# Kernel tuning notes

Measured on AMD Instinct MI355X. Metric: run time of the kernel, lower is better.

## Reference

```python
import jax, jax.numpy as jnp
import numpy as np

B, T, CODE_NUM, MED_NUM = 256, 32, 4880, 1000
CODE_SIZE, H, OUT = 128, 128, 4880


def setup_inputs() -> dict:
    key = jax.random.key(0)
    ks = jax.random.split(key, 16)
    code_x = (jax.random.uniform(ks[0], (B, T, CODE_NUM)) < 0.05).astype(jnp.float32)
    medicine_codes = (jax.random.uniform(ks[1], (B, T, MED_NUM)) < 0.02).astype(jnp.float32)
    divided = (jax.random.uniform(ks[2], (B, T, CODE_NUM)) < 0.05).astype(jnp.float32)
    neighbors = (jax.random.uniform(ks[3], (B, T, CODE_NUM)) < 0.05).astype(jnp.float32)
    lens = jax.random.randint(ks[4], (B,), 1, T + 1)
    s = lambda fan: 1.0 / np.sqrt(fan)
    c_emb = jax.random.normal(ks[5], (CODE_NUM, CODE_SIZE)) * s(CODE_SIZE)
    m_emb = jax.random.normal(ks[6], (MED_NUM, CODE_SIZE)) * s(CODE_SIZE)
    W_c = jax.random.normal(ks[7], (CODE_SIZE, H)) * s(CODE_SIZE)
    W_m = jax.random.normal(ks[8], (CODE_SIZE, H)) * s(CODE_SIZE)
    Wa = jax.random.normal(ks[9], (3 * H, 32)) * s(3 * H)
    ba = jnp.zeros((32,), jnp.float32)
    va = jax.random.normal(ks[10], (32,)) * s(32)
    W_cls = jax.random.normal(ks[11], (3 * H, OUT)) * s(3 * H)
    b_cls = jnp.zeros((OUT,), jnp.float32)
    return dict(code_x=code_x, divided=divided, neighbors=neighbors, lens=lens,
                medicine_codes=medicine_codes, c_emb=c_emb, m_emb=m_emb,
                W_c=W_c, W_m=W_m, Wa=Wa, ba=ba, va=va, W_cls=W_cls, b_cls=b_cls)


def _forward(code_x, medicine_codes, lens, c_emb, m_emb, W_c, W_m, Wa, ba, va, W_cls, b_cls):
    # hypergraph_part: transform code/med embeddings, aggregate active codes per visit
    Hc = jnp.tanh(c_emb @ W_c)                      # [code_num, H]
    Hm = jnp.tanh(m_emb @ W_m)                      # [med_num, H]
    sum_c = jnp.einsum('btc,ch->bth', code_x, Hc)   # masked sum over active dx codes
    sum_m = jnp.einsum('btm,mh->bth', medicine_codes, Hm)
    h_c = sum_c / jnp.clip(code_x.sum(-1, keepdims=True), 1.0, None)
    h_m = sum_m / jnp.clip(medicine_codes.sum(-1, keepdims=True), 1.0, None)
    repre = jnp.concatenate([h_c, h_m, h_c * h_m], axis=-1)  # [B,T,3H]
    # DotProductAttention over visits, masked by lens
    scores = jnp.einsum('btk,k->bt', jnp.tanh(repre @ Wa + ba), va)
    mask = jnp.arange(T)[None, :] < lens[:, None]
    attn = jax.nn.softmax(jnp.where(mask, scores, -1e9), axis=-1)
    ctx = jnp.einsum('bt,btd->bd', attn, repre)     # [B,3H]
    # Classifier (dropout=identity in eval) + sigmoid
    return jax.nn.sigmoid(ctx @ W_cls + b_cls)      # [B,OUT]


def reference(code_x, divided, neighbors, lens, medicine_codes, c_emb, m_emb,
              W_c, W_m, Wa, ba, va, W_cls, b_cls):
    # divided/neighbors feed the transition branch whose output is unused
    # in the original forward's final prediction path.
    return _forward(code_x, medicine_codes, lens, c_emb, m_emb,
                    W_c, W_m, Wa, ba, va, W_cls, b_cls)
```

## Files before the change

kernel.cpp:

```cpp
#include <hip/hip_runtime.h>
#include <hip/hip_bf16.h>
#include <math.h>

#define Bsz 256
#define Tn 32
#define CODEN 4880
#define MEDN 1000
#define Hdim 128
#define OUTN 4880
#define BT (Bsz*Tn)
#define R3H 384

__global__ __launch_bounds__(128) void k_emb(
    const float* __restrict__ c_emb, const float* __restrict__ m_emb,
    const float* __restrict__ W_c, const float* __restrict__ W_m,
    float* __restrict__ Hc, float* __restrict__ Hm) {
  int row = blockIdx.x;
  const float* emb; const float* W; float* out;
  if (row < CODEN) { emb = c_emb + (size_t)row * Hdim; W = W_c; out = Hc + (size_t)row * Hdim; }
  else { int r = row - CODEN; emb = m_emb + (size_t)r * Hdim; W = W_m; out = Hm + (size_t)r * Hdim; }
  __shared__ float e[Hdim];
  int h = threadIdx.x;
  e[h] = emb[h];
  __syncthreads();
  float acc = 0.f;
#pragma unroll 8
  for (int k = 0; k < Hdim; ++k) acc += e[k] * W[k * Hdim + h];
  out[h] = tanhf(acc);
}

#define MAXC 1024
#define MAXM 256

__global__ __launch_bounds__(256) void k_visit(
    const float* __restrict__ code_x, const float* __restrict__ med,
    const float* __restrict__ Hc, const float* __restrict__ Hm,
    const float* __restrict__ Wa, const float* __restrict__ ba,
    const float* __restrict__ va,
    float* __restrict__ repre, float* __restrict__ scores) {
  int bt = blockIdx.x;
  int tid = threadIdx.x;
  __shared__ int list_c[MAXC];
  __shared__ int list_m[MAXM];
  __shared__ int cnt_c, cnt_m;
  __shared__ float rep_s[R3H];
  __shared__ float red[256];
  if (tid == 0) { cnt_c = 0; cnt_m = 0; }
  __syncthreads();

  const float4* cx = (const float4*)(code_x + (size_t)bt * CODEN);
  for (int i = tid; i < CODEN / 4; i += 256) {
    float4 v = cx[i];
    if (v.x != 0.f) { int p = atomicAdd(&cnt_c, 1); if (p < MAXC) list_c[p] = 4*i; }
    if (v.y != 0.f) { int p = atomicAdd(&cnt_c, 1); if (p < MAXC) list_c[p] = 4*i+1; }
    if (v.z != 0.f) { int p = atomicAdd(&cnt_c, 1); if (p < MAXC) list_c[p] = 4*i+2; }
    if (v.w != 0.f) { int p = atomicAdd(&cnt_c, 1); if (p < MAXC) list_c[p] = 4*i+3; }
  }
  const float4* mx = (const float4*)(med + (size_t)bt * MEDN);
  for (int i = tid; i < MEDN / 4; i += 256) {
    float4 v = mx[i];
    if (v.x != 0.f) { int p = atomicAdd(&cnt_m, 1); if (p < MAXM) list_m[p] = 4*i; }
    if (v.y != 0.f) { int p = atomicAdd(&cnt_m, 1); if (p < MAXM) list_m[p] = 4*i+1; }
    if (v.z != 0.f) { int p = atomicAdd(&cnt_m, 1); if (p < MAXM) list_m[p] = 4*i+2; }
    if (v.w != 0.f) { int p = atomicAdd(&cnt_m, 1); if (p < MAXM) list_m[p] = 4*i+3; }
  }
  __syncthreads();
  int nc = cnt_c < MAXC ? cnt_c : MAXC;
  int nm = cnt_m < MAXM ? cnt_m : MAXM;

  int h = tid & 127, half = tid >> 7;
  float accC = 0.f;
#pragma unroll 2
  for (int j = half; j < nc; j += 2) accC += Hc[(size_t)list_c[j] * Hdim + h];
  float accM = 0.f;
#pragma unroll 2
  for (int j = half; j < nm; j += 2) accM += Hm[(size_t)list_m[j] * Hdim + h];

  red[tid] = accC;
  __syncthreads();
  float hc = 0.f, hm = 0.f;
  if (half == 0) hc = (red[h] + red[h + 128]) / fmaxf((float)nc, 1.f);
  __syncthreads();
  red[tid] = accM;
  __syncthreads();
  if (half == 0) {
    hm = (red[h] + red[h + 128]) / fmaxf((float)nm, 1.f);
    rep_s[h] = hc;
    rep_s[Hdim + h] = hm;
    rep_s[2 * Hdim + h] = hc * hm;
  }
  __syncthreads();

  float* rp = repre + (size_t)bt * R3H;
  for (int i = tid; i < R3H; i += 256) rp[i] = rep_s[i];

  int j = tid & 31, kc = tid >> 5;
  float p = 0.f;
  int k0 = kc * 48;
#pragma unroll 8
  for (int k = k0; k < k0 + 48; ++k) p += rep_s[k] * Wa[k * 32 + j];
  __syncthreads();
  red[tid] = p;
  __syncthreads();
  if (tid < 32) {
    float tot = 0.f;
#pragma unroll
    for (int c = 0; c < 8; ++c) tot += red[c * 32 + tid];
    float u = tanhf(tot + ba[tid]);
    float sv = u * va[tid];
#pragma unroll
    for (int off = 16; off >= 1; off >>= 1) sv += __shfl_down(sv, off, 32);
    if (tid == 0) scores[bt] = sv;
  }
}

__global__ __launch_bounds__(128) void k_ctx(
    const float* __restrict__ scores, const int* __restrict__ lens,
    const float* __restrict__ repre, float* __restrict__ ctx) {
  int b = blockIdx.x, tid = threadIdx.x;
  __shared__ float attn[Tn];
  int len = lens[b];
  if (tid < Tn) {
    float s = scores[b * Tn + tid];
    bool valid = tid < len;
    float sm = valid ? s : -1e30f;
    float m = sm;
#pragma unroll
    for (int off = 16; off >= 1; off >>= 1) m = fmaxf(m, __shfl_xor(m, off, 32));
    float e = valid ? expf(sm - m) : 0.f;
    float sum = e;
#pragma unroll
    for (int off = 16; off >= 1; off >>= 1) sum += __shfl_xor(sum, off, 32);
    attn[tid] = e / sum;
  }
  __syncthreads();
  const float* rp = repre + (size_t)b * Tn * R3H;
  for (int d = tid; d < R3H; d += 128) {
    float a = 0.f;
#pragma unroll
    for (int t = 0; t < Tn; ++t) a += attn[t] * rp[t * R3H + d];
    ctx[(size_t)b * R3H + d] = a;
  }
}

#define FMA4(A, s, w) { A.x += (s)*(w).x; A.y += (s)*(w).y; A.z += (s)*(w).z; A.w += (s)*(w).w; }

__global__ __launch_bounds__(256) void k_cls(
    const float* __restrict__ ctx, const float* __restrict__ W_cls,
    const float* __restrict__ b_cls, float* __restrict__ out) {
  __shared__ float cs_t[R3H * 8];
  int tid = threadIdx.x;
  int ob = blockIdx.x % 5;
  int b0 = (blockIdx.x / 5) * 8;
  for (int i = tid; i < R3H * 8; i += 256) {
    int k = i >> 3, r = i & 7;
    cs_t[i] = ctx[(size_t)(b0 + r) * R3H + k];
  }
  __syncthreads();
  int o0 = ob * 1024 + tid * 4;
  if (o0 >= OUTN) return;
  float4 acc[8];
#pragma unroll
  for (int r = 0; r < 8; ++r) acc[r] = make_float4(0.f, 0.f, 0.f, 0.f);
  const float* wp = W_cls + o0;
#pragma unroll 2
  for (int k = 0; k < R3H; ++k) {
    float4 w = *(const float4*)(wp + (size_t)k * OUTN);
    float4 cA = *(const float4*)&cs_t[k * 8];
    float4 cB = *(const float4*)&cs_t[k * 8 + 4];
    FMA4(acc[0], cA.x, w); FMA4(acc[1], cA.y, w);
    FMA4(acc[2], cA.z, w); FMA4(acc[3], cA.w, w);
    FMA4(acc[4], cB.x, w); FMA4(acc[5], cB.y, w);
    FMA4(acc[6], cB.z, w); FMA4(acc[7], cB.w, w);
  }
  float4 bc = *(const float4*)(b_cls + o0);
#pragma unroll
  for (int r = 0; r < 8; ++r) {
    float4 v;
    v.x = 1.f / (1.f + expf(-(acc[r].x + bc.x)));
    v.y = 1.f / (1.f + expf(-(acc[r].y + bc.y)));
    v.z = 1.f / (1.f + expf(-(acc[r].z + bc.z)));
    v.w = 1.f / (1.f + expf(-(acc[r].w + bc.w)));
    *(float4*)(out + (size_t)(b0 + r) * OUTN + o0) = v;
  }
}

extern "C" void kernel_launch(void* const* d_in, const int* in_sizes, int n_in,
                              void* d_out, int out_size, void* d_ws, size_t ws_size,
                              hipStream_t stream) {
  const float* code_x = (const float*)d_in[0];
  const int*   lens   = (const int*)d_in[3];
  const float* med    = (const float*)d_in[4];
  const float* c_emb  = (const float*)d_in[5];
  const float* m_emb  = (const float*)d_in[6];
  const float* W_c    = (const float*)d_in[7];
  const float* W_m    = (const float*)d_in[8];
  const float* Wa     = (const float*)d_in[9];
  const float* ba     = (const float*)d_in[10];
  const float* va     = (const float*)d_in[11];
  const float* W_cls  = (const float*)d_in[12];
  const float* b_cls  = (const float*)d_in[13];
  float* out = (float*)d_out;
  float* ws  = (float*)d_ws;

  float* Hc     = ws;
  float* Hm     = ws + 624640;
  float* repre  = ws + 752640;
  float* scores = ws + 3898368;
  float* ctx    = ws + 3906560;

  hipLaunchKernelGGL(k_emb,   dim3(CODEN + MEDN), dim3(128), 0, stream,
                     c_emb, m_emb, W_c, W_m, Hc, Hm);
  hipLaunchKernelGGL(k_visit, dim3(BT), dim3(256), 0, stream,
                     code_x, med, Hc, Hm, Wa, ba, va, repre, scores);
  hipLaunchKernelGGL(k_ctx,   dim3(Bsz), dim3(128), 0, stream,
                     scores, lens, repre, ctx);
  hipLaunchKernelGGL(k_cls,   dim3(160), dim3(256), 0, stream,
                     ctx, W_cls, b_cls, out);
}
```

Measured before the change: 606.5 us.

## Replace sparse gather aggregation with fused bf16 MFMA dense GEMM per batch

Instead of building per-visit active-index lists and gathering Hc/Hm rows, each batch block computes code_x @ Hc and med @ Hm as dense bf16 MFMA GEMMs. The transposed bf16 embedding tiles are double-buffered through LDS with global_load_lds. The visit representation, attention scores, softmax and context are fused into the same kernel, which drops the repre/scores round-trip and the separate ctx kernel. The classifier loop also batches eight weight loads per step. This trades the sparsity exploitation for dense matrix-core throughput. Precision drops to bf16 for Hc/Hm, and only 256 blocks of one wave-group each run, so occupancy is limited.

```diff
diff --git a/kernel.cpp b/kernel.cpp
--- a/kernel.cpp
+++ b/kernel.cpp
@@ -8,142 +8,221 @@
 #define MEDN 1000
 #define Hdim 128
 #define OUTN 4880
-#define BT (Bsz*Tn)
 #define R3H 384
+#define KC_PAD 4896
+#define KM_PAD 1024
+#define NSC 153
+#define NSM 32
+
+typedef unsigned short u16;
+typedef __attribute__((ext_vector_type(4))) float f32x4;
+typedef __attribute__((ext_vector_type(8))) short s16x8;
+typedef __attribute__((ext_vector_type(4))) unsigned int u32x4;
+
+union PKU { u32x4 u; s16x8 s; };
+
+__device__ inline unsigned f2bf(float f) {
+  unsigned u = __float_as_uint(f);
+  return (u + 0x7fffu + ((u >> 16) & 1u)) >> 16;
+}
+__device__ inline unsigned pack2(float f0, float f1) {
+  return (__float_as_uint(f0) >> 16) | (__float_as_uint(f1) & 0xffff0000u);
+}
 
 __global__ __launch_bounds__(128) void k_emb(
     const float* __restrict__ c_emb, const float* __restrict__ m_emb,
     const float* __restrict__ W_c, const float* __restrict__ W_m,
-    float* __restrict__ Hc, float* __restrict__ Hm) {
-  int row = blockIdx.x;
-  const float* emb; const float* W; float* out;
-  if (row < CODEN) { emb = c_emb + (size_t)row * Hdim; W = W_c; out = Hc + (size_t)row * Hdim; }
-  else { int r = row - CODEN; emb = m_emb + (size_t)r * Hdim; W = W_m; out = Hm + (size_t)r * Hdim; }
+    u16* __restrict__ HcT, u16* __restrict__ HmT) {
+  int blk = blockIdx.x, h = threadIdx.x;
+  bool is_med = blk >= KC_PAD;
+  int c = is_med ? blk - KC_PAD : blk;
+  int n = is_med ? MEDN : CODEN;
+  u16* dst = is_med ? (HmT + (size_t)h * KM_PAD + c) : (HcT + (size_t)h * KC_PAD + c);
+  if (c >= n) { *dst = 0; return; }
+  const float* emb = (is_med ? m_emb : c_emb) + (size_t)c * Hdim;
+  const float* W = is_med ? W_m : W_c;
   __shared__ float e[Hdim];
-  int h = threadIdx.x;
   e[h] = emb[h];
   __syncthreads();
   float acc = 0.f;
 #pragma unroll 8
   for (int k = 0; k < Hdim; ++k) acc += e[k] * W[k * Hdim + h];
-  out[h] = tanhf(acc);
-}
-
-#define MAXC 1024
-#define MAXM 256
-
-__global__ __launch_bounds__(256) void k_visit(
+  *dst = (u16)f2bf(tanhf(acc));
+}
+
+__device__ inline void stageB(const u16* __restrict__ Bt, int k0, int ldk,
+                              u16* buf, int ttid) {
+#pragma unroll
+  for (int it = 0; it < 4; ++it) {
+    int c = it * 128 + ttid;
+    const u16* src = Bt + (size_t)(c & 127) * ldk + k0 + (c >> 7) * 8;
+#if __has_builtin(__builtin_amdgcn_global_load_lds)
+    __builtin_amdgcn_global_load_lds(
+        (const __attribute__((address_space(1))) void*)src,
+        (__attribute__((address_space(3))) void*)(buf + c * 8), 16, 0, 0);
+#else
+    *(u32x4*)(buf + c * 8) = *(const u32x4*)src;
+#endif
+  }
+}
+
+__device__ inline void loadA(const float* __restrict__ Arow, int kb, int kmax,
+                             float4& a0, float4& a1) {
+  if (kb < kmax) {
+    a0 = *(const float4*)(Arow + kb);
+    a1 = *(const float4*)(Arow + kb + 4);
+  } else {
+    a0 = make_float4(0.f, 0.f, 0.f, 0.f);
+    a1 = a0;
+  }
+}
+
+__global__ __launch_bounds__(256, 1) void k_agg(
     const float* __restrict__ code_x, const float* __restrict__ med,
-    const float* __restrict__ Hc, const float* __restrict__ Hm,
+    const u16* __restrict__ HcT, const u16* __restrict__ HmT,
     const float* __restrict__ Wa, const float* __restrict__ ba,
-    const float* __restrict__ va,
-    float* __restrict__ repre, float* __restrict__ scores) {
-  int bt = blockIdx.x;
+    const float* __restrict__ va, const int* __restrict__ lens,
+    float* __restrict__ ctx) {
+  __shared__ u16 Bc[2][4096];
+  __shared__ u16 Bm[2][4096];
+  __shared__ float Wa_s[R3H * 32];
+  __shared__ float rep_s[Tn][R3H + 4];
+  __shared__ float sc_s[Tn];
+  __shared__ float at_s[Tn];
+
+  int b = blockIdx.x;
   int tid = threadIdx.x;
-  __shared__ int list_c[MAXC];
-  __shared__ int list_m[MAXM];
-  __shared__ int cnt_c, cnt_m;
-  __shared__ float rep_s[R3H];
-  __shared__ float red[256];
-  if (tid == 0) { cnt_c = 0; cnt_m = 0; }
-  __syncthreads();
-
-  const float4* cx = (const float4*)(code_x + (size_t)bt * CODEN);
-  for (int i = tid; i < CODEN / 4; i += 256) {
-    float4 v = cx[i];
-    if (v.x != 0.f) { int p = atomicAdd(&cnt_c, 1); if (p < MAXC) list_c[p] = 4*i; }
-    if (v.y != 0.f) { int p = atomicAdd(&cnt_c, 1); if (p < MAXC) list_c[p] = 4*i+1; }
-    if (v.z != 0.f) { int p = atomicAdd(&cnt_c, 1); if (p < MAXC) list_c[p] = 4*i+2; }
-    if (v.w != 0.f) { int p = atomicAdd(&cnt_c, 1); if (p < MAXC) list_c[p] = 4*i+3; }
-  }
-  const float4* mx = (const float4*)(med + (size_t)bt * MEDN);
-  for (int i = tid; i < MEDN / 4; i += 256) {
-    float4 v = mx[i];
-    if (v.x != 0.f) { int p = atomicAdd(&cnt_m, 1); if (p < MAXM) list_m[p] = 4*i; }
-    if (v.y != 0.f) { int p = atomicAdd(&cnt_m, 1); if (p < MAXM) list_m[p] = 4*i+1; }
-    if (v.z != 0.f) { int p = atomicAdd(&cnt_m, 1); if (p < MAXM) list_m[p] = 4*i+2; }
-    if (v.w != 0.f) { int p = atomicAdd(&cnt_m, 1); if (p < MAXM) list_m[p] = 4*i+3; }
-  }
-  __syncthreads();
-  int nc = cnt_c < MAXC ? cnt_c : MAXC;
-  int nm = cnt_m < MAXM ? cnt_m : MAXM;
-
-  int h = tid & 127, half = tid >> 7;
-  float accC = 0.f;
-#pragma unroll 2
-  for (int j = half; j < nc; j += 2) accC += Hc[(size_t)list_c[j] * Hdim + h];
-  float accM = 0.f;
-#pragma unroll 2
-  for (int j = half; j < nm; j += 2) accM += Hm[(size_t)list_m[j] * Hdim + h];
-
-  red[tid] = accC;
-  __syncthreads();
-  float hc = 0.f, hm = 0.f;
-  if (half == 0) hc = (red[h] + red[h + 128]) / fmaxf((float)nc, 1.f);
-  __syncthreads();
-  red[tid] = accM;
-  __syncthreads();
-  if (half == 0) {
-    hm = (red[h] + red[h + 128]) / fmaxf((float)nm, 1.f);
-    rep_s[h] = hc;
-    rep_s[Hdim + h] = hm;
-    rep_s[2 * Hdim + h] = hc * hm;
-  }
-  __syncthreads();
-
-  float* rp = repre + (size_t)bt * R3H;
-  for (int i = tid; i < R3H; i += 256) rp[i] = rep_s[i];
-
-  int j = tid & 31, kc = tid >> 5;
-  float p = 0.f;
-  int k0 = kc * 48;
-#pragma unroll 8
-  for (int k = k0; k < k0 + 48; ++k) p += rep_s[k] * Wa[k * 32 + j];
-  __syncthreads();
-  red[tid] = p;
-  __syncthreads();
-  if (tid < 32) {
-    float tot = 0.f;
-#pragma unroll
-    for (int c = 0; c < 8; ++c) tot += red[c * 32 + tid];
-    float u = tanhf(tot + ba[tid]);
-    float sv = u * va[tid];
-#pragma unroll
-    for (int off = 16; off >= 1; off >>= 1) sv += __shfl_down(sv, off, 32);
-    if (tid == 0) scores[bt] = sv;
-  }
-}
-
-__global__ __launch_bounds__(128) void k_ctx(
-    const float* __restrict__ scores, const int* __restrict__ lens,
-    const float* __restrict__ repre, float* __restrict__ ctx) {
-  int b = blockIdx.x, tid = threadIdx.x;
-  __shared__ float attn[Tn];
-  int len = lens[b];
+  int l = tid & 63;
+  int l15 = l & 15, sub = l >> 4;
+  bool codes_team = tid < 128;
+  int ttid = codes_team ? tid : tid - 128;
+  int twid = ttid >> 6;
+  int trow = twid * 16 + l15;
+
+  {
+    const float4* s4 = (const float4*)Wa;
+    float4* d4 = (float4*)Wa_s;
+    for (int i = tid; i < R3H * 32 / 4; i += 256) d4[i] = s4[i];
+  }
+
+  f32x4 acc[8];
+#pragma unroll
+  for (int f = 0; f < 8; ++f) acc[f] = (f32x4){0.f, 0.f, 0.f, 0.f};
+  float cnt = 0.f;
+
+  const float* Arow;
+  const u16* Bt;
+  u16 *buf0, *buf1;
+  int NS, kmax, ldk;
+  if (codes_team) {
+    Arow = code_x + (size_t)(b * Tn + trow) * CODEN;
+    Bt = HcT; buf0 = Bc[0]; buf1 = Bc[1]; NS = NSC; kmax = CODEN; ldk = KC_PAD;
+  } else {
+    Arow = med + (size_t)(b * Tn + trow) * MEDN;
+    Bt = HmT; buf0 = Bm[0]; buf1 = Bm[1]; NS = NSM; kmax = MEDN; ldk = KM_PAD;
+  }
+
+  float4 a0, a1;
+  float4 n0 = make_float4(0.f, 0.f, 0.f, 0.f), n1 = n0;
+  stageB(Bt, 0, ldk, buf0, ttid);
+  loadA(Arow, sub * 8, kmax, a0, a1);
+
+  for (int s = 0; s < NSC; ++s) {
+    __syncthreads();
+    bool active = s < NS;
+    bool nxt = (s + 1) < NS;
+    if (nxt) {
+      stageB(Bt, (s + 1) * 32, ldk, ((s + 1) & 1) ? buf1 : buf0, ttid);
+      loadA(Arow, (s + 1) * 32 + sub * 8, kmax, n0, n1);
+    }
+    if (active) {
+      cnt += a0.x + a0.y + a0.z + a0.w + a1.x + a1.y + a1.z + a1.w;
+      PKU pa;
+      pa.u[0] = pack2(a0.x, a0.y);
+      pa.u[1] = pack2(a0.z, a0.w);
+      pa.u[2] = pack2(a1.x, a1.y);
+      pa.u[3] = pack2(a1.z, a1.w);
+      const u16* bb = ((s & 1) ? buf1 : buf0) + sub * 1024;
+#pragma unroll
+      for (int f = 0; f < 8; ++f) {
+        PKU pb;
+        pb.u = *(const u32x4*)(bb + (f * 16 + l15) * 8);
+        acc[f] = __builtin_amdgcn_mfma_f32_16x16x32_bf16(pa.s, pb.s, acc[f], 0, 0, 0);
+      }
+      a0 = n0; a1 = n1;
+    }
+  }
+
+  cnt += __shfl_xor(cnt, 16, 64);
+  cnt += __shfl_xor(cnt, 32, 64);
+
+  int cbase = codes_team ? 0 : 128;
+#pragma unroll
+  for (int j = 0; j < 4; ++j) {
+    int r = sub * 4 + j;
+    float cr = __shfl(cnt, r, 64);
+    float iv = 1.0f / fmaxf(cr, 1.0f);
+    int t = twid * 16 + r;
+#pragma unroll
+    for (int f = 0; f < 8; ++f)
+      rep_s[t][cbase + f * 16 + l15] = acc[f][j] * iv;
+  }
+  __syncthreads();
+
+  for (int i = tid; i < Tn * 128; i += 256) {
+    int t = i >> 7, c = i & 127;
+    rep_s[t][256 + c] = rep_s[t][c] * rep_s[t][128 + c];
+  }
+  __syncthreads();
+
+  {
+    int t = tid >> 3, j0 = (tid & 7) * 4;
+    float u0 = 0.f, u1 = 0.f, u2 = 0.f, u3 = 0.f;
+    for (int k = 0; k < R3H; ++k) {
+      float r = rep_s[t][k];
+      u0 += r * Wa_s[k * 32 + j0];
+      u1 += r * Wa_s[k * 32 + j0 + 1];
+      u2 += r * Wa_s[k * 32 + j0 + 2];
+      u3 += r * Wa_s[k * 32 + j0 + 3];
+    }
+    float sv = tanhf(u0 + ba[j0])     * va[j0]
+             + tanhf(u1 + ba[j0 + 1]) * va[j0 + 1]
+             + tanhf(u2 + ba[j0 + 2]) * va[j0 + 2]
+             + tanhf(u3 + ba[j0 + 3]) * va[j0 + 3];
+    sv += __shfl_xor(sv, 1, 64);
+    sv += __shfl_xor(sv, 2, 64);
+    sv += __shfl_xor(sv, 4, 64);
+    if ((tid & 7) == 0) sc_s[t] = sv;
+  }
+  __syncthreads();
+
   if (tid < Tn) {
-    float s = scores[b * Tn + tid];
+    int len = lens[b];
+    float s = sc_s[tid];
     bool valid = tid < len;
     float sm = valid ? s : -1e30f;
     float m = sm;
 #pragma unroll
     for (int off = 16; off >= 1; off >>= 1) m = fmaxf(m, __shfl_xor(m, off, 32));
     float e = valid ? expf(sm - m) : 0.f;
-    float sum = e;
-#pragma unroll
-    for (int off = 16; off >= 1; off >>= 1) sum += __shfl_xor(sum, off, 32);
-    attn[tid] = e / sum;
-  }
-  __syncthreads();
-  const float* rp = repre + (size_t)b * Tn * R3H;
-  for (int d = tid; d < R3H; d += 128) {
+    float su = e;
+#pragma unroll
+    for (int off = 16; off >= 1; off >>= 1) su += __shfl_xor(su, off, 32);
+    at_s[tid] = e / su;
+  }
+  __syncthreads();
+
+  for (int d = tid; d < R3H; d += 256) {
     float a = 0.f;
 #pragma unroll
-    for (int t = 0; t < Tn; ++t) a += attn[t] * rp[t * R3H + d];
+    for (int t = 0; t < Tn; ++t) a += at_s[t] * rep_s[t][d];
     ctx[(size_t)b * R3H + d] = a;
   }
 }
 
-#define FMA4(A, s, w) { A.x += (s)*(w).x; A.y += (s)*(w).y; A.z += (s)*(w).z; A.w += (s)*(w).w; }
+__device__ inline void fma4(float4& a, float s, const float4& w) {
+  a.x += s * w.x; a.y += s * w.y; a.z += s * w.z; a.w += s * w.w;
+}
 
 __global__ __launch_bounds__(256) void k_cls(
     const float* __restrict__ ctx, const float* __restrict__ W_cls,
@@ -163,15 +242,19 @@
 #pragma unroll
   for (int r = 0; r < 8; ++r) acc[r] = make_float4(0.f, 0.f, 0.f, 0.f);
   const float* wp = W_cls + o0;
-#pragma unroll 2
-  for (int k = 0; k < R3H; ++k) {
-    float4 w = *(const float4*)(wp + (size_t)k * OUTN);
-    float4 cA = *(const float4*)&cs_t[k * 8];
-    float4 cB = *(const float4*)&cs_t[k * 8 + 4];
-    FMA4(acc[0], cA.x, w); FMA4(acc[1], cA.y, w);
-    FMA4(acc[2], cA.z, w); FMA4(acc[3], cA.w, w);
-    FMA4(acc[4], cB.x, w); FMA4(acc[5], cB.y, w);
-    FMA4(acc[6], cB.z, w); FMA4(acc[7], cB.w, w);
+  for (int k = 0; k < R3H; k += 8) {
+    float4 wv[8];
+#pragma unroll
+    for (int u = 0; u < 8; ++u) wv[u] = *(const float4*)(wp + (size_t)(k + u) * OUTN);
+#pragma unroll
+    for (int u = 0; u < 8; ++u) {
+      float4 cA = *(const float4*)&cs_t[(k + u) * 8];
+      float4 cB = *(const float4*)&cs_t[(k + u) * 8 + 4];
+      fma4(acc[0], cA.x, wv[u]); fma4(acc[1], cA.y, wv[u]);
+      fma4(acc[2], cA.z, wv[u]); fma4(acc[3], cA.w, wv[u]);
+      fma4(acc[4], cB.x, wv[u]); fma4(acc[5], cB.y, wv[u]);
+      fma4(acc[6], cB.z, wv[u]); fma4(acc[7], cB.w, wv[u]);
+    }
   }
   float4 bc = *(const float4*)(b_cls + o0);
 #pragma unroll
@@ -201,20 +284,15 @@
   const float* W_cls  = (const float*)d_in[12];
   const float* b_cls  = (const float*)d_in[13];
   float* out = (float*)d_out;
-  float* ws  = (float*)d_ws;
-
-  float* Hc     = ws;
-  float* Hm     = ws + 624640;
-  float* repre  = ws + 752640;
-  float* scores = ws + 3898368;
-  float* ctx    = ws + 3906560;
-
-  hipLaunchKernelGGL(k_emb,   dim3(CODEN + MEDN), dim3(128), 0, stream,
-                     c_emb, m_emb, W_c, W_m, Hc, Hm);
-  hipLaunchKernelGGL(k_visit, dim3(BT), dim3(256), 0, stream,
-                     code_x, med, Hc, Hm, Wa, ba, va, repre, scores);
-  hipLaunchKernelGGL(k_ctx,   dim3(Bsz), dim3(128), 0, stream,
-                     scores, lens, repre, ctx);
-  hipLaunchKernelGGL(k_cls,   dim3(160), dim3(256), 0, stream,
+
+  u16* HcT   = (u16*)d_ws;
+  u16* HmT   = HcT + (size_t)128 * KC_PAD;
+  float* ctx = (float*)(HmT + (size_t)128 * KM_PAD);
+
+  hipLaunchKernelGGL(k_emb, dim3(KC_PAD + KM_PAD), dim3(128), 0, stream,
+                     c_emb, m_emb, W_c, W_m, HcT, HmT);
+  hipLaunchKernelGGL(k_agg, dim3(Bsz), dim3(256), 0, stream,
+                     code_x, med, HcT, HmT, Wa, ba, va, lens, ctx);
+  hipLaunchKernelGGL(k_cls, dim3(160), dim3(256), 0, stream,
                      ctx, W_cls, b_cls, out);
 }
```

Measured after the change: 642.7 us. +6.0%, slower.
